# Performance work log

Hardware: AMD Instinct MI355X
Metric: run time of the kernel (lower is better)

## Reference

```python
import jax, jax.numpy as jnp
import numpy as np


def setup_inputs() -> dict:
    key = jax.random.key(0)
    k1, k2, k3 = jax.random.split(key, 3)
    B, C, E = 65536, 32, 512
    candidate_ids = jax.random.randint(k1, (B, C), 0, E, dtype=jnp.int64)
    candidate_scores = jax.random.uniform(k2, (B, C), dtype=jnp.float32)
    cooc = jax.random.uniform(k3, (E, E), dtype=jnp.float32)
    # row-normalize like update_cooccurrence would maintain
    cooc = cooc / jnp.clip(cooc.sum(axis=1, keepdims=True), 1e-8)
    return {
        "candidate_ids": candidate_ids,
        "candidate_scores": candidate_scores,
        "cooccurrence": cooc,
        "target_size": 64,
    }


def reference(candidate_ids, candidate_scores, cooccurrence, target_size):
    B, C = candidate_ids.shape
    E = cooccurrence.shape[0]
    num_to_add = target_size - C  # static; original returns early if <= 0
    rows = jnp.arange(B)[:, None]  # [B,1]
    # sum_i score[b,i] * cooccurrence[ids[b,i]]  ==  scatter scores into [B,E], then matmul
    sparse_scores = jnp.zeros((B, E), jnp.float32).at[rows, candidate_ids].add(candidate_scores)
    cooc_scores = sparse_scores @ cooccurrence  # [B,E]
    # mask out existing candidates
    cooc_scores = cooc_scores.at[rows, candidate_ids].set(-jnp.inf)
    additional_scores, additional_ids = jax.lax.top_k(cooc_scores, num_to_add)
    expanded_ids = jnp.concatenate([candidate_ids, additional_ids.astype(candidate_ids.dtype)], axis=-1)
    expanded_scores = jnp.concatenate([candidate_scores, additional_scores], axis=-1)
    return expanded_ids, expanded_scores
```

## Files before the change

### kernel.cpp

```cpp
#include <hip/hip_runtime.h>
#include <stdint.h>

typedef unsigned long long u64;
typedef unsigned int u32;
typedef float vf2 __attribute__((ext_vector_type(2)));

constexpr int Ccand = 32;
constexpr int Evoc  = 512;
constexpr int Tgt   = 64;

__device__ __forceinline__ void sort64_desc_f32(float& a, int lane) {
    #pragma unroll
    for (int k2 = 2; k2 <= 64; k2 <<= 1) {
        #pragma unroll
        for (int j = k2 >> 1; j > 0; j >>= 1) {
            float o = __shfl_xor(a, j);
            bool lower = (lane & j) == 0;
            bool keepMax = ((lane & k2) == 0) ? lower : !lower;
            bool g = a > o;
            a = (keepMax == g) ? a : o;
        }
    }
}

__device__ __forceinline__ void sort64_desc_u64(u64& a, int lane) {
    #pragma unroll
    for (int k2 = 2; k2 <= 64; k2 <<= 1) {
        #pragma unroll
        for (int j = k2 >> 1; j > 0; j >>= 1) {
            u64 o = __shfl_xor(a, j);
            bool lower = (lane & j) == 0;
            bool keepMax = ((lane & k2) == 0) ? lower : !lower;
            bool g = a > o;
            a = (keepMax == g) ? a : o;
        }
    }
}

__global__ __launch_bounds__(256, 8) void cooc_expand(
    const int* __restrict__ cand_ids,
    const float* __restrict__ cand_scores,
    const float* __restrict__ cooc,
    float* __restrict__ out_ids,
    float* __restrict__ out_scores,
    int B)
{
    const int lane = threadIdx.x & 63;
    const int wid  = threadIdx.x >> 6;
    const int row  = blockIdx.x * 4 + wid;
    __shared__ u64 buf[4][64];
    if (row >= B) return;

    int   my_id = -1;
    float my_s  = 0.0f;
    if (lane < Ccand) {
        my_id = cand_ids[(size_t)row * Ccand + lane];
        my_s  = cand_scores[(size_t)row * Ccand + lane];
    }

    int   first = 64;
    float sm    = 0.0f;
    #pragma unroll
    for (int j = 0; j < Ccand; ++j) {
        int   idj = __shfl(my_id, j);
        float sj  = __shfl(my_s,  j);
        bool match = (idj == my_id);
        if (match && j < first) first = j;
        sm += match ? sj : 0.0f;
    }
    bool alive = (lane < Ccand) && (first == lane);
    u64 aball = __ballot(alive);
    int m = __popcll(aball);

    int rk = 0;
    #pragma unroll
    for (int j = 0; j < Ccand; ++j) {
        int idj = __shfl(my_id, j);
        bool aj = (aball >> j) & 1ull;
        rk += (aj && idj < my_id) ? 1 : 0;
    }
    int dst = alive ? rk : ((lane < 32) ? (lane + 32) : lane);
    int sorted_id = __builtin_amdgcn_ds_permute(dst << 2, my_id);
    int sorted_sb = __builtin_amdgcn_ds_permute(dst << 2, __float_as_int(sm));

    vf2 acc2[4];
    acc2[0] = (vf2){0.f, 0.f}; acc2[1] = (vf2){0.f, 0.f};
    acc2[2] = (vf2){0.f, 0.f}; acc2[3] = (vf2){0.f, 0.f};
    u32 maskbits = 0;
    const int l4 = lane << 2;
    #pragma unroll 1
    for (int t = 0; t < 32; t += 4) {
        int   e[4];
        float s[4];
        #pragma unroll
        for (int u = 0; u < 4; ++u) {
            e[u] = __builtin_amdgcn_readlane(sorted_id, t + u) & 511;
            s[u] = (t + u < m) ? __int_as_float(__builtin_amdgcn_readlane(sorted_sb, t + u)) : 0.0f;
        }
        float4 A[4], Bv[4];
        #pragma unroll
        for (int u = 0; u < 4; ++u) {
            const float* rp = cooc + ((size_t)e[u] << 9);
            A[u]  = *reinterpret_cast<const float4*>(rp + l4);
            Bv[u] = *reinterpret_cast<const float4*>(rp + 256 + l4);
        }
        #pragma unroll
        for (int u = 0; u < 4; ++u) {
            vf2 sv2; sv2[0] = s[u]; sv2[1] = s[u];
            vf2 a0; a0[0] = A[u].x;  a0[1] = A[u].y;
            vf2 a1; a1[0] = A[u].z;  a1[1] = A[u].w;
            vf2 b0; b0[0] = Bv[u].x; b0[1] = Bv[u].y;
            vf2 b1; b1[0] = Bv[u].z; b1[1] = Bv[u].w;
            acc2[0] = __builtin_elementwise_fma(sv2, a0, acc2[0]);
            acc2[1] = __builtin_elementwise_fma(sv2, a1, acc2[1]);
            acc2[2] = __builtin_elementwise_fma(sv2, b0, acc2[2]);
            acc2[3] = __builtin_elementwise_fma(sv2, b1, acc2[3]);
        }
        #pragma unroll
        for (int u = 0; u < 4; ++u) {
            if ((t + u < m) && (((e[u] & 255) >> 2) == lane))
                maskbits |= 1u << (((e[u] >> 8) << 2) | (e[u] & 3));
        }
    }

    float v[8];
    v[0] = acc2[0][0]; v[1] = acc2[0][1]; v[2] = acc2[1][0]; v[3] = acc2[1][1];
    v[4] = acc2[2][0]; v[5] = acc2[2][1]; v[6] = acc2[3][0]; v[7] = acc2[3][1];
    #pragma unroll
    for (int j = 0; j < 8; ++j)
        if ((maskbits >> j) & 1u) v[j] = -1.0f;

    float mx8 = v[0];
    #pragma unroll
    for (int j = 1; j < 8; ++j) mx8 = fmaxf(mx8, v[j]);
    float srt = mx8;
    sort64_desc_f32(srt, lane);
    float L32 = __int_as_float(__builtin_amdgcn_readlane(__float_as_int(srt), 31));

    int cnt = 0;
    #pragma unroll
    for (int j = 0; j < 8; ++j) cnt += (v[j] >= L32) ? 1 : 0;
    u32 sincl = (u32)cnt;
    #pragma unroll
    for (int i = 1; i < 64; i <<= 1) {
        u32 t2 = __shfl_up(sincl, i);
        if (lane >= i) sincl += t2;
    }
    int sbase = (int)sincl - cnt;
    int S_tot = __builtin_amdgcn_readlane((int)sincl, 63);

    int nchunk = (S_tot + 63) >> 6;
    u64 cur = 0ull;
    #pragma unroll 1
    for (int c = 0; c < nchunk; ++c) {
        const int lo = c << 6;
        int slot = sbase;
        #pragma unroll
        for (int j = 0; j < 8; ++j) {
            bool s = (v[j] >= L32);
            int  rel = slot - lo;
            if (s && rel >= 0 && rel < 64) {
                int col = (j < 4) ? (l4 + j) : (256 + l4 + (j - 4));
                buf[wid][rel] = ((u64)__float_as_uint(v[j]) << 32) | (u32)(511 - col);
            }
            slot += s ? 1 : 0;
        }
        __threadfence_block();
        u64 nxt = (lo + lane < S_tot) ? buf[wid][lane] : 0ull;
        __threadfence_block();
        sort64_desc_u64(nxt, lane);
        if (c == 0) {
            cur = nxt;
        } else {
            u64 o = __shfl_xor(nxt, 63);
            cur = (cur >= o) ? cur : o;
            #pragma unroll
            for (int j = 32; j > 0; j >>= 1) {
                u64 p = __shfl_xor(cur, j);
                bool keepMax = (lane & j) == 0;
                bool g = cur > p;
                cur = (keepMax == g) ? cur : p;
            }
        }
    }

    int src = (lane >= 32) ? (lane - 32) : 0;
    u64 kk = __shfl(cur, src);
    const size_t ob = (size_t)row * Tgt;
    float oid, osc;
    if (lane < Ccand) {
        oid = (float)my_id;
        osc = my_s;
    } else {
        oid = (float)(int)(511 - (u32)(kk & 511ull));
        osc = __uint_as_float((u32)(kk >> 32));
    }
    out_ids[ob + lane]    = oid;
    out_scores[ob + lane] = osc;
}

extern "C" void kernel_launch(void* const* d_in, const int* in_sizes, int n_in,
                              void* d_out, int out_size, void* d_ws, size_t ws_size,
                              hipStream_t stream) {
    const int*   ids    = (const int*)d_in[0];
    const float* scores = (const float*)d_in[1];
    const float* cooc   = (const float*)d_in[2];
    int B = in_sizes[0] / Ccand;
    float* out_ids    = (float*)d_out;
    float* out_scores = out_ids + (size_t)B * Tgt;
    int blocks = (B + 3) / 4;
    hipLaunchKernelGGL(cooc_expand, dim3(blocks), dim3(256), 0, stream,
                       ids, scores, cooc, out_ids, out_scores, B);
}
```

Baseline: 211.0 us.

## Use DPP/swizzle sorts, LDS candidate mask, ballot-based scans, and trip loop to unique count

Bitonic sort steps now use DPP and ds_swizzle for small lane strides in place of generic shuffles. The existing-candidate mask is built in shared memory with atomicOr, and the per-lane mask bits are read back from it. The dedup and rank loops use readlane-built bitmasks with popcount, and the prefix sum uses bitwise ballots with mbcnt. The gather loop stops at the unique-candidate count instead of always running 32 steps. Together these cut shuffle and ALU instruction count per row, at the cost of more complex and more hardware-specific code.

```diff
diff --git a/kernel.cpp b/kernel.cpp
--- a/kernel.cpp
+++ b/kernel.cpp
@@ -9,32 +9,48 @@
 constexpr int Evoc  = 512;
 constexpr int Tgt   = 64;
 
+template<int J>
+__device__ __forceinline__ int shx32(int x) {
+    if constexpr (J == 1)       return __builtin_amdgcn_update_dpp(0, x, 0xB1, 0xF, 0xF, true);
+    else if constexpr (J == 2)  return __builtin_amdgcn_update_dpp(0, x, 0x4E, 0xF, 0xF, true);
+    else if constexpr (J <= 16) return __builtin_amdgcn_ds_swizzle(x, (J << 10) | 0x1F);
+    else                        return __shfl_xor(x, J);
+}
+
+template<int K2, int J>
+__device__ __forceinline__ void cas_f32(float& a, int lane) {
+    float o = __int_as_float(shx32<J>(__float_as_int(a)));
+    bool keepMax = (((lane & K2) == 0) == ((lane & J) == 0));
+    bool g = a > o;
+    a = (keepMax == g) ? a : o;
+}
+
+template<int K2, int J>
+__device__ __forceinline__ void cas_u64(u64& a, int lane) {
+    int lo = shx32<J>((int)(u32)a);
+    int hi = shx32<J>((int)(u32)(a >> 32));
+    u64 o = ((u64)(u32)hi << 32) | (u32)lo;
+    bool keepMax = (((lane & K2) == 0) == ((lane & J) == 0));
+    bool g = a > o;
+    a = (keepMax == g) ? a : o;
+}
+
 __device__ __forceinline__ void sort64_desc_f32(float& a, int lane) {
-    #pragma unroll
-    for (int k2 = 2; k2 <= 64; k2 <<= 1) {
-        #pragma unroll
-        for (int j = k2 >> 1; j > 0; j >>= 1) {
-            float o = __shfl_xor(a, j);
-            bool lower = (lane & j) == 0;
-            bool keepMax = ((lane & k2) == 0) ? lower : !lower;
-            bool g = a > o;
-            a = (keepMax == g) ? a : o;
-        }
-    }
+    cas_f32<2,1>(a,lane);
+    cas_f32<4,2>(a,lane);   cas_f32<4,1>(a,lane);
+    cas_f32<8,4>(a,lane);   cas_f32<8,2>(a,lane);   cas_f32<8,1>(a,lane);
+    cas_f32<16,8>(a,lane);  cas_f32<16,4>(a,lane);  cas_f32<16,2>(a,lane);  cas_f32<16,1>(a,lane);
+    cas_f32<32,16>(a,lane); cas_f32<32,8>(a,lane);  cas_f32<32,4>(a,lane);  cas_f32<32,2>(a,lane);  cas_f32<32,1>(a,lane);
+    cas_f32<64,32>(a,lane); cas_f32<64,16>(a,lane); cas_f32<64,8>(a,lane);  cas_f32<64,4>(a,lane);  cas_f32<64,2>(a,lane); cas_f32<64,1>(a,lane);
 }
 
 __device__ __forceinline__ void sort64_desc_u64(u64& a, int lane) {
-    #pragma unroll
-    for (int k2 = 2; k2 <= 64; k2 <<= 1) {
-        #pragma unroll
-        for (int j = k2 >> 1; j > 0; j >>= 1) {
-            u64 o = __shfl_xor(a, j);
-            bool lower = (lane & j) == 0;
-            bool keepMax = ((lane & k2) == 0) ? lower : !lower;
-            bool g = a > o;
-            a = (keepMax == g) ? a : o;
-        }
-    }
+    cas_u64<2,1>(a,lane);
+    cas_u64<4,2>(a,lane);   cas_u64<4,1>(a,lane);
+    cas_u64<8,4>(a,lane);   cas_u64<8,2>(a,lane);   cas_u64<8,1>(a,lane);
+    cas_u64<16,8>(a,lane);  cas_u64<16,4>(a,lane);  cas_u64<16,2>(a,lane);  cas_u64<16,1>(a,lane);
+    cas_u64<32,16>(a,lane); cas_u64<32,8>(a,lane);  cas_u64<32,4>(a,lane);  cas_u64<32,2>(a,lane);  cas_u64<32,1>(a,lane);
+    cas_u64<64,32>(a,lane); cas_u64<64,16>(a,lane); cas_u64<64,8>(a,lane);  cas_u64<64,4>(a,lane);  cas_u64<64,2>(a,lane); cas_u64<64,1>(a,lane);
 }
 
 __global__ __launch_bounds__(256, 8) void cooc_expand(
@@ -49,36 +65,37 @@
     const int wid  = threadIdx.x >> 6;
     const int row  = blockIdx.x * 4 + wid;
     __shared__ u64 buf[4][64];
+    __shared__ u32 maskw[4][16];
     if (row >= B) return;
 
+    if (lane < 16) maskw[wid][lane] = 0u;
     int   my_id = -1;
     float my_s  = 0.0f;
     if (lane < Ccand) {
         my_id = cand_ids[(size_t)row * Ccand + lane];
         my_s  = cand_scores[(size_t)row * Ccand + lane];
     }
-
-    int   first = 64;
-    float sm    = 0.0f;
+    __threadfence_block();
+    if (lane < Ccand)
+        atomicOr(&maskw[wid][(u32)my_id >> 5], 1u << (my_id & 31));
+
+    u32 eqm = 0, ltm = 0;
+    float sm = 0.0f;
     #pragma unroll
     for (int j = 0; j < Ccand; ++j) {
-        int   idj = __shfl(my_id, j);
-        float sj  = __shfl(my_s,  j);
-        bool match = (idj == my_id);
-        if (match && j < first) first = j;
-        sm += match ? sj : 0.0f;
-    }
-    bool alive = (lane < Ccand) && (first == lane);
+        int   idj = __builtin_amdgcn_readlane(my_id, j);
+        float sj  = __int_as_float(__builtin_amdgcn_readlane(__float_as_int(my_s), j));
+        bool eq = (idj == my_id);
+        eqm |= eq ? (1u << j) : 0u;
+        ltm |= (idj < my_id) ? (1u << j) : 0u;
+        sm  += eq ? sj : 0.0f;
+    }
+    u32 below = (1u << (lane & 31)) - 1u;
+    bool alive = (lane < Ccand) && ((eqm & below) == 0u);
     u64 aball = __ballot(alive);
-    int m = __popcll(aball);
-
-    int rk = 0;
-    #pragma unroll
-    for (int j = 0; j < Ccand; ++j) {
-        int idj = __shfl(my_id, j);
-        bool aj = (aball >> j) & 1ull;
-        rk += (aj && idj < my_id) ? 1 : 0;
-    }
+    int m  = __popcll(aball);
+    int rk = __popc(ltm & (u32)aball);
+
     int dst = alive ? rk : ((lane < 32) ? (lane + 32) : lane);
     int sorted_id = __builtin_amdgcn_ds_permute(dst << 2, my_id);
     int sorted_sb = __builtin_amdgcn_ds_permute(dst << 2, __float_as_int(sm));
@@ -86,16 +103,17 @@
     vf2 acc2[4];
     acc2[0] = (vf2){0.f, 0.f}; acc2[1] = (vf2){0.f, 0.f};
     acc2[2] = (vf2){0.f, 0.f}; acc2[3] = (vf2){0.f, 0.f};
-    u32 maskbits = 0;
     const int l4 = lane << 2;
     #pragma unroll 1
-    for (int t = 0; t < 32; t += 4) {
+    for (int t = 0; t < m; t += 4) {
         int   e[4];
         float s[4];
         #pragma unroll
         for (int u = 0; u < 4; ++u) {
-            e[u] = __builtin_amdgcn_readlane(sorted_id, t + u) & 511;
-            s[u] = (t + u < m) ? __int_as_float(__builtin_amdgcn_readlane(sorted_sb, t + u)) : 0.0f;
+            int idx  = t + u;
+            int idxc = (idx < m) ? idx : (m - 1);
+            e[u] = __builtin_amdgcn_readlane(sorted_id, idxc) & 511;
+            s[u] = (idx < m) ? __int_as_float(__builtin_amdgcn_readlane(sorted_sb, idx)) : 0.0f;
         }
         float4 A[4], Bv[4];
         #pragma unroll
@@ -116,19 +134,20 @@
             acc2[2] = __builtin_elementwise_fma(sv2, b0, acc2[2]);
             acc2[3] = __builtin_elementwise_fma(sv2, b1, acc2[3]);
         }
-        #pragma unroll
-        for (int u = 0; u < 4; ++u) {
-            if ((t + u < m) && (((e[u] & 255) >> 2) == lane))
-                maskbits |= 1u << (((e[u] >> 8) << 2) | (e[u] & 3));
-        }
-    }
+    }
+
+    __threadfence_block();
+    u32 wA = maskw[wid][lane >> 3];
+    u32 wB = maskw[wid][8 + (lane >> 3)];
+    int sh = (lane & 7) << 2;
+    u32 mb = ((wA >> sh) & 15u) | (((wB >> sh) & 15u) << 4);
 
     float v[8];
     v[0] = acc2[0][0]; v[1] = acc2[0][1]; v[2] = acc2[1][0]; v[3] = acc2[1][1];
     v[4] = acc2[2][0]; v[5] = acc2[2][1]; v[6] = acc2[3][0]; v[7] = acc2[3][1];
     #pragma unroll
     for (int j = 0; j < 8; ++j)
-        if ((maskbits >> j) & 1u) v[j] = -1.0f;
+        if ((mb >> j) & 1u) v[j] = -1.0f;
 
     float mx8 = v[0];
     #pragma unroll
@@ -140,14 +159,15 @@
     int cnt = 0;
     #pragma unroll
     for (int j = 0; j < 8; ++j) cnt += (v[j] >= L32) ? 1 : 0;
-    u32 sincl = (u32)cnt;
-    #pragma unroll
-    for (int i = 1; i < 64; i <<= 1) {
-        u32 t2 = __shfl_up(sincl, i);
-        if (lane >= i) sincl += t2;
-    }
-    int sbase = (int)sincl - cnt;
-    int S_tot = __builtin_amdgcn_readlane((int)sincl, 63);
+    int sbase = 0, S_tot = 0;
+    #pragma unroll
+    for (int b = 0; b < 4; ++b) {
+        u64 bal = __ballot(((cnt >> b) & 1) != 0);
+        int pc = __builtin_amdgcn_mbcnt_hi((u32)(bal >> 32),
+                 __builtin_amdgcn_mbcnt_lo((u32)bal, 0));
+        sbase += pc << b;
+        S_tot += ((int)__popcll(bal)) << b;
+    }
 
     int nchunk = (S_tot + 63) >> 6;
     u64 cur = 0ull;
@@ -174,13 +194,12 @@
         } else {
             u64 o = __shfl_xor(nxt, 63);
             cur = (cur >= o) ? cur : o;
-            #pragma unroll
-            for (int j = 32; j > 0; j >>= 1) {
-                u64 p = __shfl_xor(cur, j);
-                bool keepMax = (lane & j) == 0;
-                bool g = cur > p;
-                cur = (keepMax == g) ? cur : p;
-            }
+            cas_u64<64,32>(cur, lane);
+            cas_u64<64,16>(cur, lane);
+            cas_u64<64,8>(cur, lane);
+            cas_u64<64,4>(cur, lane);
+            cas_u64<64,2>(cur, lane);
+            cas_u64<64,1>(cur, lane);
         }
     }
 
```

After: 206.0 us. 1.02x faster.
